# Kernel optimization log

Hardware: AMD Instinct MI355X
Metric: run time of the kernel (lower is better)

## Reference

```python
import jax, jax.numpy as jnp
from jax import lax
import numpy as np

DIM = 384
HEADS = 8
SR = 2
B, D0, D1, D2 = 4, 16, 16, 16
N = 1 + D0 * D1 * D2


def setup_inputs() -> dict:
    key = jax.random.key(0)
    ks = jax.random.split(key, 8)
    s = 0.02
    return {
        "x": jax.random.normal(ks[0], (B, N, DIM), dtype=jnp.float32),
        "q_w": jax.random.normal(ks[1], (DIM, DIM), dtype=jnp.float32) * s,
        "kv_w": jax.random.normal(ks[2], (2 * DIM, DIM), dtype=jnp.float32) * s,
        "proj_w": jax.random.normal(ks[3], (DIM, DIM), dtype=jnp.float32) * s,
        "proj_b": jnp.zeros((DIM,), dtype=jnp.float32),
        "sr_w": jax.random.normal(ks[4], (DIM, 1, SR, SR, SR), dtype=jnp.float32) * s,  # depthwise (groups=dim)
        "sr_b": jnp.zeros((DIM,), dtype=jnp.float32),
        "ln_g": jnp.ones((DIM,), dtype=jnp.float32),
        "ln_b": jnp.zeros((DIM,), dtype=jnp.float32),
        "d0": D0, "d1": D1, "d2": D2,
    }


def reference(x, q_w, kv_w, proj_w, proj_b, sr_w, sr_b, ln_g, ln_b, d0, d1, d2):
    B_, N_, C = x.shape
    hd = C // HEADS
    scale = hd ** -0.5

    # q projection -> [B, H, N, hd]
    q = (x @ q_w.T).reshape(B_, N_, HEADS, hd).transpose(0, 2, 1, 3)

    # spatial reduction of patch tokens (keep CLS token)
    x_ = x[:, 1:].transpose(0, 2, 1).reshape(B_, C, d0, d1, d2)
    x_ = lax.conv_general_dilated(
        x_, sr_w, window_strides=(SR, SR, SR), padding="VALID",
        dimension_numbers=("NCDHW", "OIDHW", "NCDHW"), feature_group_count=C,
    ) + sr_b[None, :, None, None, None]
    x_ = x_.reshape(B_, C, -1).transpose(0, 2, 1)           # [B, M-1, C]
    x_ = jnp.concatenate([x[:, 0:1], x_], axis=1)            # [B, M, C]

    # LayerNorm (eps=1e-5)
    mu = jnp.mean(x_, axis=-1, keepdims=True)
    var = jnp.var(x_, axis=-1, keepdims=True)
    x_ = (x_ - mu) / jnp.sqrt(var + 1e-5) * ln_g + ln_b

    M = x_.shape[1]
    kv = (x_ @ kv_w.T).reshape(B_, M, 2, HEADS, hd).transpose(2, 0, 3, 1, 4)
    k, v = kv[0], kv[1]                                      # [B, H, M, hd]

    attn = jax.nn.softmax(jnp.einsum("bhnd,bhmd->bhnm", q, k) * scale, axis=-1)
    out = jnp.einsum("bhnm,bhmd->bhnd", attn, v)
    out = out.transpose(0, 2, 1, 3).reshape(B_, N_, C)
    return out @ proj_w.T + proj_b
```

## Files before the change

kernel.cpp:

```cpp
#include <hip/hip_runtime.h>

typedef unsigned short u16;
typedef unsigned int u32;
typedef __bf16 bf16x8 __attribute__((ext_vector_type(8)));
typedef float f32x4 __attribute__((ext_vector_type(4)));

#define NTOK 4097
#define MTOK 513
#define MPAD 544
#define KPAD 640
#define NPAD_Q 4224
#define ROWS_X 16512

__device__ __forceinline__ u16 f2bf(float f) {
  u32 u = __builtin_bit_cast(u32, f);
  u = u + 0x7FFFu + ((u >> 16) & 1u);
  return (u16)(u >> 16);
}
__device__ __forceinline__ u16 f2bf_fast(float f) {
  u32 u = __builtin_bit_cast(u32, f);
  return (u16)((u + 0x8000u) >> 16);
}

__device__ __forceinline__ void gld16(const u16* g, u16* l) {
  __builtin_amdgcn_global_load_lds((const __attribute__((address_space(1))) u32*)g,
                                   (__attribute__((address_space(3))) u32*)l, 16, 0, 0);
}

#define NX   6292992
#define NQW  147456
#define NKVW 294912
#define NPW  147456
#define GX   (NX / 8)
#define GQW  (NQW / 8)
#define GKVW (NKVW / 8)
#define GPW  (NPW / 8)
#define GTOT (GX + GQW + GKVW + GPW)
#define SRLN_BLOCKS (4 * MTOK)

__global__ void pre_kernel(const float* __restrict__ x, const float* __restrict__ qw,
                           const float* __restrict__ kvw, const float* __restrict__ pw,
                           const float* __restrict__ srw, const float* __restrict__ srb,
                           const float* __restrict__ lng, const float* __restrict__ lnb,
                           u16* __restrict__ xb, u16* __restrict__ qwb,
                           u16* __restrict__ kvwb, u16* __restrict__ pwb,
                           u16* __restrict__ xln) {
  if (blockIdx.x < SRLN_BLOCKS) {
    int c = threadIdx.x;
    int bm = blockIdx.x;
    int b = bm / MTOK, m = bm - b * MTOK;
    float v;
    if (m == 0) {
      v = x[(b * NTOK) * 384 + c];
    } else {
      int mo = m - 1;
      int oz = mo >> 6, oy = (mo >> 3) & 7, ox = mo & 7;
      float acc = srb[c];
#pragma unroll
      for (int dz = 0; dz < 2; dz++)
#pragma unroll
        for (int dy = 0; dy < 2; dy++)
#pragma unroll
          for (int dx = 0; dx < 2; dx++) {
            int tok = 1 + ((2 * oz + dz) * 256 + (2 * oy + dy) * 16 + (2 * ox + dx));
            acc += x[(b * NTOK + tok) * 384 + c] * srw[c * 8 + dz * 4 + dy * 2 + dx];
          }
      v = acc;
    }
    float s1 = v, s2 = v * v;
#pragma unroll
    for (int msk = 32; msk >= 1; msk >>= 1) {
      s1 += __shfl_xor(s1, msk);
      s2 += __shfl_xor(s2, msk);
    }
    __shared__ float r1[6], r2[6];
    int w = threadIdx.x >> 6, lane = threadIdx.x & 63;
    if (lane == 0) { r1[w] = s1; r2[w] = s2; }
    __syncthreads();
    float S1 = 0.f, S2 = 0.f;
#pragma unroll
    for (int i = 0; i < 6; i++) { S1 += r1[i]; S2 += r2[i]; }
    float mu = S1 * (1.0f / 384.0f);
    float var = S2 * (1.0f / 384.0f) - mu * mu;
    float y = (v - mu) * rsqrtf(var + 1e-5f) * lng[c] + lnb[c];
    xln[(b * MPAD + m) * 384 + c] = f2bf(y);
  } else {
    int idx = (blockIdx.x - SRLN_BLOCKS) * blockDim.x + threadIdx.x;
    int stride = (gridDim.x - SRLN_BLOCKS) * blockDim.x;
    for (int g = idx; g < GTOT; g += stride) {
      const float* s;
      u16* d;
      int off;
      if (g < GX) { s = x; d = xb; off = g * 8; }
      else if (g < GX + GQW) { s = qw; d = qwb; off = (g - GX) * 8; }
      else if (g < GX + GQW + GKVW) { s = kvw; d = kvwb; off = (g - GX - GQW) * 8; }
      else { s = pw; d = pwb; off = (g - GX - GQW - GKVW) * 8; }
      float4 v0 = *(const float4*)(s + off);
      float4 v1 = *(const float4*)(s + off + 4);
      uint4 o;
      u16* p = (u16*)&o;
      p[0] = f2bf(v0.x); p[1] = f2bf(v0.y); p[2] = f2bf(v0.z); p[3] = f2bf(v0.w);
      p[4] = f2bf(v1.x); p[5] = f2bf(v1.y); p[6] = f2bf(v1.z); p[7] = f2bf(v1.w);
      *(uint4*)(d + off) = o;
    }
  }
}

__device__ __forceinline__ void gemm_core(u16* aLds, u16* bLds,
                                          const u16* __restrict__ A, const u16* __restrict__ W,
                                          int mode, size_t rbase, int c0,
                                          u16* __restrict__ o1, u16* __restrict__ o2,
                                          float* __restrict__ of, const float* __restrict__ bias) {
  int tid = threadIdx.x, w = tid >> 6, lane = tid & 63, q4 = lane >> 4, c16 = lane & 15;
  int wr = w >> 1, wc = w & 1;
  int x7 = c16 & 7;

  auto stageAB = [&](int kc, int buf) {
#pragma unroll
    for (int i = 0; i < 4; i++) {
      int s = (w * 4 + i) * 64 + lane;
      int row = s >> 3, chp = s & 7;
      int ch = chp ^ (row & 7);
      gld16(A + (rbase + row) * 384 + kc * 64 + ch * 8, &aLds[buf * 8192 + (w * 4 + i) * 512]);
    }
#pragma unroll
    for (int i = 0; i < 4; i++) {
      int s = (w * 4 + i) * 64 + lane;
      int row = s >> 3, chp = s & 7;
      int ch = chp ^ (row & 7);
      gld16(W + (size_t)(c0 + row) * 384 + kc * 64 + ch * 8, &bLds[buf * 8192 + (w * 4 + i) * 512]);
    }
  };
  stageAB(0, 0);
  __syncthreads();

  f32x4 acc[4][4];
#pragma unroll
  for (int mt = 0; mt < 4; mt++)
#pragma unroll
    for (int nt = 0; nt < 4; nt++) acc[mt][nt] = (f32x4){0, 0, 0, 0};

  for (int c = 0; c < 6; c++) {
    int cb = c & 1, nb = cb ^ 1;
    if (c < 5) stageAB(c + 1, nb);
#pragma unroll
    for (int ks = 0; ks < 2; ks++) {
      bf16x8 af[4], bf[4];
#pragma unroll
      for (int mt = 0; mt < 4; mt++)
        af[mt] = *(const bf16x8*)(&aLds[cb * 8192 + (wr * 64 + mt * 16 + c16) * 64 + ((ks * 4 + q4) ^ x7) * 8]);
#pragma unroll
      for (int nt = 0; nt < 4; nt++)
        bf[nt] = *(const bf16x8*)(&bLds[cb * 8192 + (wc * 64 + nt * 16 + c16) * 64 + ((ks * 4 + q4) ^ x7) * 8]);
#pragma unroll
      for (int mt = 0; mt < 4; mt++)
#pragma unroll
        for (int nt = 0; nt < 4; nt++)
          acc[mt][nt] = __builtin_amdgcn_mfma_f32_16x16x32_bf16(af[mt], bf[nt], acc[mt][nt], 0, 0, 0);
    }
    __syncthreads();
  }

#pragma unroll
  for (int mt = 0; mt < 4; mt++)
#pragma unroll
    for (int nt = 0; nt < 4; nt++) {
      int col = c0 + wc * 64 + nt * 16 + c16;
#pragma unroll
      for (int r = 0; r < 4; r++) {
        int R = (int)rbase + wr * 64 + mt * 16 + q4 * 4 + r;
        float val = acc[mt][nt][r];
        if (mode == 0) {
          int b = R / NTOK;
          if (b >= 4) continue;
          int n = R - b * NTOK;
          int h = col / 48, d = col - h * 48;
          o1[((size_t)(b * 8 + h) * NPAD_Q + n) * 64 + d] = f2bf(val * 0.14433756729740643f);
        } else if (mode == 1) {
          int b = R / MPAD;
          int m = R - b * MPAD;
          if (col < 384) {
            int h = col / 48, d = col - h * 48;
            o1[((size_t)(b * 8 + h) * KPAD + m) * 64 + d] = f2bf(val);
          } else {
            int c2 = col - 384;
            int h = c2 / 48, d = c2 - h * 48;
            o2[((size_t)(b * 8 + h) * 48 + d) * KPAD + m] = f2bf(val);
          }
        } else {
          if (R < 4 * NTOK) of[(size_t)R * 384 + col] = val + bias[col];
        }
      }
    }
}

__global__ __launch_bounds__(256) void gemm_qkv(const u16* __restrict__ xb, const u16* __restrict__ qwb,
                                                const u16* __restrict__ xlnb, const u16* __restrict__ kvwb,
                                                u16* __restrict__ qb, u16* __restrict__ kb2,
                                                u16* __restrict__ vtb) {
  __shared__ __align__(16) u16 aLds[2 * 128 * 64];
  __shared__ __align__(16) u16 bLds[2 * 128 * 64];
  int bx = blockIdx.x;
  if (bx < 387) {
    gemm_core(aLds, bLds, xb, qwb, 0, (size_t)(bx % 129) * 128, (bx / 129) * 128,
              qb, nullptr, nullptr, nullptr);
  } else {
    int i = bx - 387;
    gemm_core(aLds, bLds, xlnb, kvwb, 1, (size_t)(i % 17) * 128, (i / 17) * 128,
              kb2, vtb, nullptr, nullptr);
  }
}

__global__ __launch_bounds__(256) void gemm_out(const u16* __restrict__ A, const u16* __restrict__ W,
                                                float* __restrict__ of, const float* __restrict__ bias) {
  __shared__ __align__(16) u16 aLds[2 * 128 * 64];
  __shared__ __align__(16) u16 bLds[2 * 128 * 64];
  gemm_core(aLds, bLds, A, W, 2, (size_t)blockIdx.x * 128, blockIdx.y * 128,
            nullptr, nullptr, of, bias);
}

__global__ __launch_bounds__(256, 4) void attn_kernel(const u16* __restrict__ qb,
                                                      const u16* __restrict__ kb,
                                                      const u16* __restrict__ vt,
                                                      u16* __restrict__ outb) {
  __shared__ __align__(16) u16 klds[2][64][64];
  __shared__ __align__(16) u16 vlds[2][48][64];
  __shared__ __align__(16) u16 plds[4][16][76];
  int tid = threadIdx.x, w = tid >> 6, lane = tid & 63, q4 = lane >> 4, c16 = lane & 15;
  int bh = blockIdx.x;
  int n0 = blockIdx.y * 128 + w * 32;
  int r7 = c16 & 7;

  const uint4* qp = (const uint4*)(qb + ((size_t)bh * NPAD_Q + n0 + c16) * 64);
  bf16x8 aq[2][2];
#pragma unroll
  for (int rg = 0; rg < 2; rg++) {
    aq[rg][0] = __builtin_bit_cast(bf16x8, qp[rg * 128 + q4]);
    aq[rg][1] = __builtin_bit_cast(bf16x8, qp[rg * 128 + 4 + q4]);
  }

  const u16* kbase = kb + (size_t)bh * KPAD * 64;
  const u16* vbase = vt + (size_t)bh * 48 * KPAD;

  auto stage = [&](int cn, int buf) {
#pragma unroll
    for (int i = 0; i < 2; i++) {
      int s = (w * 2 + i) * 64 + lane;
      int row = s >> 3, chp = s & 7;
      int ch = chp ^ (row & 7);
      gld16(kbase + (size_t)(cn * 64 + row) * 64 + ch * 8, &klds[buf][(w * 2 + i) * 8][0]);
    }
#pragma unroll
    for (int i = 0; i < 2; i++) {
      int blk = w * 2 + i;
      if (blk < 6) {
        int s = blk * 64 + lane;
        int row = s >> 3, chp = s & 7;
        int ch = chp ^ (row & 7);
        gld16(vbase + (size_t)row * KPAD + cn * 64 + ch * 8, &vlds[buf][blk * 8][0]);
      }
    }
  };

  stage(0, 0);
  __syncthreads();

  f32x4 o[2][3];
  float lsum[2][4];
#pragma unroll
  for (int rg = 0; rg < 2; rg++) {
#pragma unroll
    for (int nt = 0; nt < 3; nt++) o[rg][nt] = (f32x4){0, 0, 0, 0};
#pragma unroll
    for (int r = 0; r < 4; r++) lsum[rg][r] = 0.f;
  }

  for (int c = 0; c < 8; c++) {
    int cb = c & 1, nb = cb ^ 1;
    stage(c + 1, nb);

    f32x4 s[2][4];
#pragma unroll
    for (int rg = 0; rg < 2; rg++)
#pragma unroll
      for (int t = 0; t < 4; t++) s[rg][t] = (f32x4){0, 0, 0, 0};
#pragma unroll
    for (int t = 0; t < 4; t++) {
      const u16* krow = &klds[cb][t * 16 + c16][0];
      bf16x8 k0 = *(const bf16x8*)(krow + (q4 ^ r7) * 8);
      bf16x8 k1 = *(const bf16x8*)(krow + ((q4 ^ r7) ^ 4) * 8);
#pragma unroll
      for (int rg = 0; rg < 2; rg++) {
        s[rg][t] = __builtin_amdgcn_mfma_f32_16x16x32_bf16(aq[rg][0], k0, s[rg][t], 0, 0, 0);
        s[rg][t] = __builtin_amdgcn_mfma_f32_16x16x32_bf16(aq[rg][1], k1, s[rg][t], 0, 0, 0);
      }
    }
#pragma unroll
    for (int rg = 0; rg < 2; rg++)
#pragma unroll
      for (int t = 0; t < 4; t++)
#pragma unroll
        for (int r = 0; r < 4; r++) {
          float e = __expf(s[rg][t][r]);
          s[rg][t][r] = e;
          lsum[rg][r] += e;
        }
    bf16x8 afrag[2][2];
#pragma unroll
    for (int rg = 0; rg < 2; rg++) {
#pragma unroll
      for (int t = 0; t < 4; t++)
#pragma unroll
        for (int r = 0; r < 4; r++) plds[w][q4 * 4 + r][t * 16 + c16] = f2bf_fast(s[rg][t][r]);
#pragma unroll
      for (int kl = 0; kl < 2; kl++)
        afrag[rg][kl] = *(const bf16x8*)(&plds[w][c16][kl * 32 + q4 * 8]);
    }
#pragma unroll
    for (int kl = 0; kl < 2; kl++)
#pragma unroll
      for (int nt = 0; nt < 3; nt++) {
        const u16* vrow = &vlds[cb][nt * 16 + c16][0];
        bf16x8 bv = *(const bf16x8*)(vrow + ((kl * 4 + q4) ^ r7) * 8);
#pragma unroll
        for (int rg = 0; rg < 2; rg++)
          o[rg][nt] = __builtin_amdgcn_mfma_f32_16x16x32_bf16(afrag[rg][kl], bv, o[rg][nt], 0, 0, 0);
      }
    __syncthreads();
  }

  {
    f32x4 s4[2] = {{0, 0, 0, 0}, {0, 0, 0, 0}};
    const u16* krow = &klds[0][c16][0];
    bf16x8 k0 = *(const bf16x8*)(krow + (q4 ^ r7) * 8);
    bf16x8 k1 = *(const bf16x8*)(krow + ((q4 ^ r7) ^ 4) * 8);
#pragma unroll
    for (int rg = 0; rg < 2; rg++) {
      s4[rg] = __builtin_amdgcn_mfma_f32_16x16x32_bf16(aq[rg][0], k0, s4[rg], 0, 0, 0);
      s4[rg] = __builtin_amdgcn_mfma_f32_16x16x32_bf16(aq[rg][1], k1, s4[rg], 0, 0, 0);
    }
    bf16x8 afrag[2];
#pragma unroll
    for (int rg = 0; rg < 2; rg++) {
#pragma unroll
      for (int r = 0; r < 4; r++) {
        float e = (c16 == 0) ? __expf(s4[rg][r]) : 0.f;
        lsum[rg][r] += e;
        plds[w][q4 * 4 + r][c16] = f2bf_fast(e);
        plds[w][q4 * 4 + r][16 + c16] = 0;
      }
      afrag[rg] = *(const bf16x8*)(&plds[w][c16][q4 * 8]);
    }
#pragma unroll
    for (int nt = 0; nt < 3; nt++) {
      const u16* vrow = &vlds[0][nt * 16 + c16][0];
      bf16x8 bv = *(const bf16x8*)(vrow + (q4 ^ r7) * 8);
#pragma unroll
      for (int rg = 0; rg < 2; rg++)
        o[rg][nt] = __builtin_amdgcn_mfma_f32_16x16x32_bf16(afrag[rg], bv, o[rg][nt], 0, 0, 0);
    }
  }

  int b = bh >> 3, h = bh & 7;
#pragma unroll
  for (int rg = 0; rg < 2; rg++) {
    float inv[4];
#pragma unroll
    for (int r = 0; r < 4; r++) {
      float l = lsum[rg][r];
      l += __shfl_xor(l, 1);
      l += __shfl_xor(l, 2);
      l += __shfl_xor(l, 4);
      l += __shfl_xor(l, 8);
      inv[r] = 1.0f / l;
    }
#pragma unroll
    for (int nt = 0; nt < 3; nt++)
#pragma unroll
      for (int r = 0; r < 4; r++) {
        int n = n0 + rg * 16 + q4 * 4 + r;
        if (n < NTOK) outb[((size_t)(b * NTOK + n)) * 384 + h * 48 + nt * 16 + c16] = f2bf(o[rg][nt][r] * inv[r]);
      }
  }
}

extern "C" void kernel_launch(void* const* d_in, const int* in_sizes, int n_in,
                              void* d_out, int out_size, void* d_ws, size_t ws_size,
                              hipStream_t stream) {
  const float* x = (const float*)d_in[0];
  const float* q_w = (const float*)d_in[1];
  const float* kv_w = (const float*)d_in[2];
  const float* proj_w = (const float*)d_in[3];
  const float* proj_b = (const float*)d_in[4];
  const float* sr_w = (const float*)d_in[5];
  const float* sr_b = (const float*)d_in[6];
  const float* ln_g = (const float*)d_in[7];
  const float* ln_b = (const float*)d_in[8];
  float* out = (float*)d_out;

  u16* ws = (u16*)d_ws;
  u16* x_b = ws;
  u16* qw_b = x_b + (size_t)ROWS_X * 384;
  u16* kvw_b = qw_b + 147456;
  u16* pw_b = kvw_b + 294912;
  u16* q_b = pw_b + 147456;
  u16* xln_b = q_b + (size_t)32 * NPAD_Q * 64;
  u16* k_b = xln_b + (size_t)4 * MPAD * 384;
  u16* vt_b = k_b + (size_t)32 * KPAD * 64;
  u16* attn_b = x_b;


  pre_kernel<<<SRLN_BLOCKS + 2240, 384, 0, stream>>>(x, q_w, kv_w, proj_w, sr_w, sr_b,
                                                     ln_g, ln_b, x_b, qw_b, kvw_b, pw_b, xln_b);
  gemm_qkv<<<489, 256, 0, stream>>>(x_b, qw_b, xln_b, kvw_b, q_b, k_b, vt_b);
  attn_kernel<<<dim3(32, 33), 256, 0, stream>>>(q_b, k_b, vt_b, attn_b);
  gemm_out<<<dim3(129, 3), 256, 0, stream>>>(attn_b, pw_b, out, proj_b);
}
```

Before: 179.0 us.

## Fuse fp32-to-bf16 cast of x into Q GEMM A-tile staging

Removes the separate pass that converted all of x to bf16. The Q-projection GEMM now loads fp32 x straight into registers, converts it, and writes it to LDS, and it runs in the same launch as the spatial-reduction/LayerNorm blocks. Weight casting moves to a small dedicated kernel, and the KV GEMM becomes its own launch. This saves a full write and re-read of x in bf16, but the A operand is now staged through registers instead of async global-to-LDS loads, 128 threads per GEMM block sit idle, and there is one extra launch.

```diff
diff --git a/kernel.cpp b/kernel.cpp
--- a/kernel.cpp
+++ b/kernel.cpp
@@ -27,27 +27,152 @@
                                    (__attribute__((address_space(3))) u32*)l, 16, 0, 0);
 }
 
-#define NX   6292992
 #define NQW  147456
 #define NKVW 294912
 #define NPW  147456
-#define GX   (NX / 8)
 #define GQW  (NQW / 8)
 #define GKVW (NKVW / 8)
 #define GPW  (NPW / 8)
-#define GTOT (GX + GQW + GKVW + GPW)
 #define SRLN_BLOCKS (4 * MTOK)
 
-__global__ void pre_kernel(const float* __restrict__ x, const float* __restrict__ qw,
-                           const float* __restrict__ kvw, const float* __restrict__ pw,
-                           const float* __restrict__ srw, const float* __restrict__ srb,
-                           const float* __restrict__ lng, const float* __restrict__ lnb,
-                           u16* __restrict__ xb, u16* __restrict__ qwb,
-                           u16* __restrict__ kvwb, u16* __restrict__ pwb,
-                           u16* __restrict__ xln) {
-  if (blockIdx.x < SRLN_BLOCKS) {
+__global__ void wcast_kernel(const float* __restrict__ qw, const float* __restrict__ kvw,
+                             const float* __restrict__ pw, u16* __restrict__ qwb,
+                             u16* __restrict__ kvwb, u16* __restrict__ pwb) {
+  const int GW = GQW + GKVW + GPW;
+  int idx = blockIdx.x * blockDim.x + threadIdx.x;
+  int stride = gridDim.x * blockDim.x;
+  for (int g = idx; g < GW; g += stride) {
+    const float* s;
+    u16* d;
+    int off;
+    if (g < GQW) { s = qw; d = qwb; off = g * 8; }
+    else if (g < GQW + GKVW) { s = kvw; d = kvwb; off = (g - GQW) * 8; }
+    else { s = pw; d = pwb; off = (g - GQW - GKVW) * 8; }
+    float4 v0 = *(const float4*)(s + off);
+    float4 v1 = *(const float4*)(s + off + 4);
+    uint4 o;
+    u16* p = (u16*)&o;
+    p[0] = f2bf(v0.x); p[1] = f2bf(v0.y); p[2] = f2bf(v0.z); p[3] = f2bf(v0.w);
+    p[4] = f2bf(v1.x); p[5] = f2bf(v1.y); p[6] = f2bf(v1.z); p[7] = f2bf(v1.w);
+    *(uint4*)(d + off) = o;
+  }
+}
+
+__global__ __launch_bounds__(384, 3) void fused_q_srln(
+    const float* __restrict__ x, const u16* __restrict__ qwb,
+    const float* __restrict__ srw, const float* __restrict__ srb,
+    const float* __restrict__ lng, const float* __restrict__ lnb,
+    u16* __restrict__ qb, u16* __restrict__ xln) {
+  __shared__ __align__(16) u16 aLds[2 * 128 * 64];
+  __shared__ __align__(16) u16 bLds[2 * 128 * 64];
+  __shared__ float r1[6], r2[6];
+  int bx = blockIdx.x;
+  if (bx < 387) {
+    int tid = threadIdx.x, w = tid >> 6, lane = tid & 63, q4 = lane >> 4, c16 = lane & 15;
+    bool act = tid < 256;
+    int wr = w >> 1, wc = w & 1;
+    int x7 = c16 & 7;
+    size_t rbase = (size_t)(bx % 129) * 128;
+    int c0 = (bx / 129) * 128;
+
+    float4 ra[4][2];
+    auto loadA = [&](int kc) {
+#pragma unroll
+      for (int i = 0; i < 4; i++) {
+        int s = (w * 4 + i) * 64 + lane;
+        int row = s >> 3, chp = s & 7;
+        int ch = chp ^ (row & 7);
+        int ar = (int)rbase + row;
+        if (ar > 16387) ar = 16387;
+        const float* pa = x + (size_t)ar * 384 + kc * 64 + ch * 8;
+        ra[i][0] = *(const float4*)pa;
+        ra[i][1] = *(const float4*)(pa + 4);
+      }
+    };
+    auto writeA = [&](int buf) {
+#pragma unroll
+      for (int i = 0; i < 4; i++) {
+        uint4 oa;
+        u16* p = (u16*)&oa;
+        p[0] = f2bf(ra[i][0].x); p[1] = f2bf(ra[i][0].y);
+        p[2] = f2bf(ra[i][0].z); p[3] = f2bf(ra[i][0].w);
+        p[4] = f2bf(ra[i][1].x); p[5] = f2bf(ra[i][1].y);
+        p[6] = f2bf(ra[i][1].z); p[7] = f2bf(ra[i][1].w);
+        *(uint4*)(&aLds[buf * 8192 + (w * 4 + i) * 512 + lane * 8]) = oa;
+      }
+    };
+    auto stageB = [&](int kc, int buf) {
+#pragma unroll
+      for (int i = 0; i < 4; i++) {
+        int s = (w * 4 + i) * 64 + lane;
+        int row = s >> 3, chp = s & 7;
+        int ch = chp ^ (row & 7);
+        gld16(qwb + (size_t)(c0 + row) * 384 + kc * 64 + ch * 8,
+              &bLds[buf * 8192 + (w * 4 + i) * 512]);
+      }
+    };
+
+    if (act) {
+      loadA(0);
+      stageB(0, 0);
+      writeA(0);
+    }
+    __syncthreads();
+
+    f32x4 acc[4][4];
+#pragma unroll
+    for (int mt = 0; mt < 4; mt++)
+#pragma unroll
+      for (int nt = 0; nt < 4; nt++) acc[mt][nt] = (f32x4){0, 0, 0, 0};
+
+    for (int c = 0; c < 6; c++) {
+      int cb = c & 1, nb = cb ^ 1;
+      if (act && c < 5) {
+        loadA(c + 1);
+        stageB(c + 1, nb);
+      }
+      if (act) {
+#pragma unroll
+        for (int ks = 0; ks < 2; ks++) {
+          bf16x8 af[4], bf[4];
+#pragma unroll
+          for (int mt = 0; mt < 4; mt++)
+            af[mt] = *(const bf16x8*)(&aLds[cb * 8192 + (wr * 64 + mt * 16 + c16) * 64 + ((ks * 4 + q4) ^ x7) * 8]);
+#pragma unroll
+          for (int nt = 0; nt < 4; nt++)
+            bf[nt] = *(const bf16x8*)(&bLds[cb * 8192 + (wc * 64 + nt * 16 + c16) * 64 + ((ks * 4 + q4) ^ x7) * 8]);
+#pragma unroll
+          for (int mt = 0; mt < 4; mt++)
+#pragma unroll
+            for (int nt = 0; nt < 4; nt++)
+              acc[mt][nt] = __builtin_amdgcn_mfma_f32_16x16x32_bf16(af[mt], bf[nt], acc[mt][nt], 0, 0, 0);
+        }
+      }
+      if (act && c < 5) writeA(nb);
+      __syncthreads();
+    }
+
+    if (act) {
+#pragma unroll
+      for (int mt = 0; mt < 4; mt++)
+#pragma unroll
+        for (int nt = 0; nt < 4; nt++) {
+          int col = c0 + wc * 64 + nt * 16 + c16;
+#pragma unroll
+          for (int r = 0; r < 4; r++) {
+            int R = (int)rbase + wr * 64 + mt * 16 + q4 * 4 + r;
+            int b = R / NTOK;
+            if (b >= 4) continue;
+            int n = R - b * NTOK;
+            int h = col / 48, d = col - h * 48;
+            qb[((size_t)(b * 8 + h) * NPAD_Q + n) * 64 + d] =
+                f2bf(acc[mt][nt][r] * 0.14433756729740643f);
+          }
+        }
+    }
+  } else {
     int c = threadIdx.x;
-    int bm = blockIdx.x;
+    int bm = bx - 387;
     int b = bm / MTOK, m = bm - b * MTOK;
     float v;
     if (m == 0) {
@@ -73,7 +198,6 @@
       s1 += __shfl_xor(s1, msk);
       s2 += __shfl_xor(s2, msk);
     }
-    __shared__ float r1[6], r2[6];
     int w = threadIdx.x >> 6, lane = threadIdx.x & 63;
     if (lane == 0) { r1[w] = s1; r2[w] = s2; }
     __syncthreads();
@@ -84,25 +208,6 @@
     float var = S2 * (1.0f / 384.0f) - mu * mu;
     float y = (v - mu) * rsqrtf(var + 1e-5f) * lng[c] + lnb[c];
     xln[(b * MPAD + m) * 384 + c] = f2bf(y);
-  } else {
-    int idx = (blockIdx.x - SRLN_BLOCKS) * blockDim.x + threadIdx.x;
-    int stride = (gridDim.x - SRLN_BLOCKS) * blockDim.x;
-    for (int g = idx; g < GTOT; g += stride) {
-      const float* s;
-      u16* d;
-      int off;
-      if (g < GX) { s = x; d = xb; off = g * 8; }
-      else if (g < GX + GQW) { s = qw; d = qwb; off = (g - GX) * 8; }
-      else if (g < GX + GQW + GKVW) { s = kvw; d = kvwb; off = (g - GX - GQW) * 8; }
-      else { s = pw; d = pwb; off = (g - GX - GQW - GKVW) * 8; }
-      float4 v0 = *(const float4*)(s + off);
-      float4 v1 = *(const float4*)(s + off + 4);
-      uint4 o;
-      u16* p = (u16*)&o;
-      p[0] = f2bf(v0.x); p[1] = f2bf(v0.y); p[2] = f2bf(v0.z); p[3] = f2bf(v0.w);
-      p[4] = f2bf(v1.x); p[5] = f2bf(v1.y); p[6] = f2bf(v1.z); p[7] = f2bf(v1.w);
-      *(uint4*)(d + off) = o;
-    }
   }
 }
 
@@ -194,21 +299,13 @@
     }
 }
 
-__global__ __launch_bounds__(256) void gemm_qkv(const u16* __restrict__ xb, const u16* __restrict__ qwb,
-                                                const u16* __restrict__ xlnb, const u16* __restrict__ kvwb,
-                                                u16* __restrict__ qb, u16* __restrict__ kb2,
-                                                u16* __restrict__ vtb) {
+__global__ __launch_bounds__(256) void gemm_kv(const u16* __restrict__ xlnb, const u16* __restrict__ kvwb,
+                                               u16* __restrict__ kb2, u16* __restrict__ vtb) {
   __shared__ __align__(16) u16 aLds[2 * 128 * 64];
   __shared__ __align__(16) u16 bLds[2 * 128 * 64];
-  int bx = blockIdx.x;
-  if (bx < 387) {
-    gemm_core(aLds, bLds, xb, qwb, 0, (size_t)(bx % 129) * 128, (bx / 129) * 128,
-              qb, nullptr, nullptr, nullptr);
-  } else {
-    int i = bx - 387;
-    gemm_core(aLds, bLds, xlnb, kvwb, 1, (size_t)(i % 17) * 128, (i / 17) * 128,
-              kb2, vtb, nullptr, nullptr);
-  }
+  int i = blockIdx.x;
+  gemm_core(aLds, bLds, xlnb, kvwb, 1, (size_t)(i % 17) * 128, (i / 17) * 128,
+            kb2, vtb, nullptr, nullptr);
 }
 
 __global__ __launch_bounds__(256) void gemm_out(const u16* __restrict__ A, const u16* __restrict__ W,
@@ -410,9 +507,9 @@
   u16* attn_b = x_b;
 
 
-  pre_kernel<<<SRLN_BLOCKS + 2240, 384, 0, stream>>>(x, q_w, kv_w, proj_w, sr_w, sr_b,
-                                                     ln_g, ln_b, x_b, qw_b, kvw_b, pw_b, xln_b);
-  gemm_qkv<<<489, 256, 0, stream>>>(x_b, qw_b, xln_b, kvw_b, q_b, k_b, vt_b);
+  wcast_kernel<<<288, 256, 0, stream>>>(q_w, kv_w, proj_w, qw_b, kvw_b, pw_b);
+  fused_q_srln<<<387 + SRLN_BLOCKS, 384, 0, stream>>>(x, qw_b, sr_w, sr_b, ln_g, ln_b, q_b, xln_b);
+  gemm_kv<<<102, 256, 0, stream>>>(xln_b, kvw_b, k_b, vt_b);
   attn_kernel<<<dim3(32, 33), 256, 0, stream>>>(q_b, k_b, vt_b, attn_b);
   gemm_out<<<dim3(129, 3), 256, 0, stream>>>(attn_b, pw_b, out, proj_b);
 }
```

After: 195.5 us. 1.09x slower.
